# Optimization experiments

Measured on AMD Instinct MI355X. Metric: run time of the kernel, lower is better.

Reference implementation:

```python
import jax, jax.numpy as jnp
import numpy as np
import math

EMBED = 64
HEADS = 2
HEAD_DIM = EMBED // HEADS
B = 262144
EPS = 1e-5


def _linear_params(key, fan_in, fan_out):
    kw, kb = jax.random.split(key)
    bound = 1.0 / math.sqrt(fan_in)
    W = jax.random.uniform(kw, (fan_out, fan_in), jnp.float32, -bound, bound)
    b = jax.random.uniform(kb, (fan_out,), jnp.float32, -bound, bound)
    return W, b


def setup_inputs() -> dict:
    key = jax.random.key(0)
    ks = jax.random.split(key, 12)
    v1 = jax.random.normal(ks[0], (B, EMBED), jnp.float32)
    v2 = jax.random.normal(ks[1], (B, EMBED), jnp.float32)
    Wq1, bq1 = _linear_params(ks[2], EMBED, EMBED)
    Wk2, bk2 = _linear_params(ks[3], EMBED, EMBED)
    Wv2, bv2 = _linear_params(ks[4], EMBED, EMBED)
    Wo1, bo1 = _linear_params(ks[5], EMBED, EMBED)
    Wq2, bq2 = _linear_params(ks[6], EMBED, EMBED)
    Wk1, bk1 = _linear_params(ks[7], EMBED, EMBED)
    Wv1, bv1 = _linear_params(ks[8], EMBED, EMBED)
    Wo2, bo2 = _linear_params(ks[9], EMBED, EMBED)
    g1 = jnp.ones((EMBED,), jnp.float32); be1 = jnp.zeros((EMBED,), jnp.float32)
    g2 = jnp.ones((EMBED,), jnp.float32); be2 = jnp.zeros((EMBED,), jnp.float32)
    return dict(v1_embed=v1, v2_embed=v2,
                Wq1=Wq1, bq1=bq1, Wk2=Wk2, bk2=bk2, Wv2=Wv2, bv2=bv2, Wo1=Wo1, bo1=bo1,
                Wq2=Wq2, bq2=bq2, Wk1=Wk1, bk1=bk1, Wv1=Wv1, bv1=bv1, Wo2=Wo2, bo2=bo2,
                g1=g1, be1=be1, g2=g2, be2=be2)


def _lin(x, W, b):
    return x @ W.T + b


def _mha_single_token(q, k, v):
    # q,k,v: (B, EMBED); one query token, one key token per batch element.
    Bq = q.shape[0]
    Q = q.reshape(Bq, HEADS, HEAD_DIM)
    K = k.reshape(Bq, HEADS, HEAD_DIM)
    V = v.reshape(Bq, HEADS, HEAD_DIM)
    scores = jnp.sum(Q * K, axis=-1, keepdims=True) / jnp.sqrt(jnp.float32(HEAD_DIM))  # (B,H,1)
    w = jax.nn.softmax(scores[..., None], axis=-1)[..., 0]  # softmax over length-1 key axis -> 1.0
    attended = w * V  # (B,H,HEAD_DIM)
    return attended.reshape(Bq, EMBED)


def _layernorm(x, g, b):
    mu = jnp.mean(x, axis=-1, keepdims=True)
    var = jnp.mean(jnp.square(x - mu), axis=-1, keepdims=True)
    return (x - mu) * jax.lax.rsqrt(var + EPS) * g + b


def reference(v1_embed, v2_embed, Wq1, bq1, Wk2, bk2, Wv2, bv2, Wo1, bo1,
              Wq2, bq2, Wk1, bk1, Wv1, bv1, Wo2, bo2, g1, be1, g2, be2):
    # v1 attends to v2
    q1p = _lin(v1_embed, Wq1, bq1)
    k2p = _lin(v2_embed, Wk2, bk2)
    v2p = _lin(v2_embed, Wv2, bv2)
    a1 = _lin(_mha_single_token(q1p, k2p, v2p), Wo1, bo1)
    a1 = _layernorm(a1 + v1_embed, g1, be1)
    # v2 attends to v1
    q2p = _lin(v2_embed, Wq2, bq2)
    k1p = _lin(v1_embed, Wk1, bk1)
    v1p = _lin(v1_embed, Wv1, bv1)
    a2 = _lin(_mha_single_token(q2p, k1p, v1p), Wo2, bo2)
    a2 = _layernorm(a2 + v2_embed, g2, be2)
    return a1, a2
```

## Files before the change

### kernel.cpp

```cpp
#include <hip/hip_runtime.h>

typedef unsigned short u16;
typedef short v8s __attribute__((ext_vector_type(8)));
typedef float f4 __attribute__((ext_vector_type(4)));

#define NROWS 262144
#define UNITS 4

__device__ __forceinline__ u16 f2bf(float f) {
  union { float f; unsigned int i; } x; x.f = f;
  unsigned int r = x.i + 0x7fffu + ((x.i >> 16) & 1u);
  return (u16)(r >> 16);
}

__global__ void fuse_weights(const float* __restrict__ Wo1, const float* __restrict__ Wv2,
                             const float* __restrict__ bv2, const float* __restrict__ bo1,
                             const float* __restrict__ Wo2, const float* __restrict__ Wv1,
                             const float* __restrict__ bv1, const float* __restrict__ bo2,
                             const float* __restrict__ g1,  const float* __restrict__ be1,
                             const float* __restrict__ g2,  const float* __restrict__ be2,
                             u16* __restrict__ M1, u16* __restrict__ M2,
                             float* __restrict__ cgb) {
  int item = blockIdx.x * 256 + threadIdx.x;
  int mat = item >> 10;
  int n   = (item >> 4) & 63;
  int k0  = (item & 15) * 4;
  const float* Wo = mat ? Wo2 : Wo1;
  const float* Wv = mat ? Wv1 : Wv2;
  float a0 = 0.f, a1 = 0.f, a2 = 0.f, a3 = 0.f;
  for (int j = 0; j < 64; ++j) {
    float w = Wo[n * 64 + j];
    f4 wv = *(const f4*)(Wv + j * 64 + k0);
    a0 += w * wv[0];
    a1 += w * wv[1];
    a2 += w * wv[2];
    a3 += w * wv[3];
  }
  u16* M = mat ? M2 : M1;
  M[n * 64 + k0 + 0] = f2bf(a0);
  M[n * 64 + k0 + 1] = f2bf(a1);
  M[n * 64 + k0 + 2] = f2bf(a2);
  M[n * 64 + k0 + 3] = f2bf(a3);
  if ((item & 15) == 0) {
    const float* bv = mat ? bv1 : bv2;
    const float* bo = mat ? bo2 : bo1;
    float s = bo[n];
    for (int j = 0; j < 64; ++j) s += Wo[n * 64 + j] * bv[j];
    cgb[mat * 64 + n] = s;
    const float* g  = mat ? g2 : g1;
    const float* be = mat ? be2 : be1;
    cgb[128 + mat * 128 + n] = g[n];
    cgb[192 + mat * 128 + n] = be[n];
  }
}

__global__ __launch_bounds__(256, 3) void xattn(
    const float* __restrict__ v1, const float* __restrict__ v2,
    const u16* __restrict__ M1, const u16* __restrict__ M2,
    const float* __restrict__ cgb,
    float* __restrict__ out1, float* __restrict__ out2) {
  const int lane = threadIdx.x & 63;
  const int wave = threadIdx.x >> 6;
  const int quad = lane >> 4;
  const int l15  = lane & 15;
  const int path = wave & 1;

  __shared__ float scgb[384];
  if (threadIdx.x < 96)
    ((f4*)scgb)[threadIdx.x] = ((const f4*)cgb)[threadIdx.x];

  const u16*   M    = path ? M2  : M1;
  const float* xsrc = path ? v1  : v2;
  const float* rsrc = path ? v2  : v1;
  float*       outp = path ? out2 : out1;
  const int coff = path * 64;
  const int goff = 128 + path * 128;
  const int boff = 192 + path * 128;

  v8s a[4][2];
#pragma unroll
  for (int mt = 0; mt < 4; ++mt)
#pragma unroll
    for (int ks = 0; ks < 2; ++ks)
      a[mt][ks] = *(const v8s*)(M + (mt * 16 + l15) * 64 + ks * 32 + quad * 8);

  const int unit0 = blockIdx.x * 2 + (wave >> 1);

  f4 x0[2], x1[2], x2[2], x3[2];
  f4 rv0[2], rv1[2], rv2[2], rv3[2];

  auto stage = [&](int buf, int tile) {
    const int rr = tile * 16;
    const float* xrow = xsrc + (size_t)(rr + l15) * 64 + quad * 8;
    x0[buf] = *(const f4*)(xrow);
    x1[buf] = *(const f4*)(xrow + 4);
    x2[buf] = *(const f4*)(xrow + 32);
    x3[buf] = *(const f4*)(xrow + 36);
    const float* rrow = rsrc + (size_t)(rr + l15) * 64 + quad * 4;
    rv0[buf] = *(const f4*)(rrow);
    rv1[buf] = *(const f4*)(rrow + 16);
    rv2[buf] = *(const f4*)(rrow + 32);
    rv3[buf] = *(const f4*)(rrow + 48);
  };

  stage(0, unit0);
  __syncthreads();

#pragma unroll
  for (int it = 0; it < UNITS; ++it) {
    const int cur = it & 1;
    const int nxt = cur ^ 1;
    const int r0 = (unit0 + it * 4096) * 16;

    if (it + 1 < UNITS) stage(nxt, unit0 + (it + 1) * 4096);

    v8s b0, b1;
#pragma unroll
    for (int j = 0; j < 4; ++j) {
      b0[j]     = (short)f2bf(x0[cur][j]);
      b0[j + 4] = (short)f2bf(x1[cur][j]);
      b1[j]     = (short)f2bf(x2[cur][j]);
      b1[j + 4] = (short)f2bf(x3[cur][j]);
    }

    f4 acc[4];
#pragma unroll
    for (int mt = 0; mt < 4; ++mt) {
      f4 c = {0.f, 0.f, 0.f, 0.f};
      c = __builtin_amdgcn_mfma_f32_16x16x32_bf16(a[mt][0], b0, c, 0, 0, 0);
      c = __builtin_amdgcn_mfma_f32_16x16x32_bf16(a[mt][1], b1, c, 0, 0, 0);
      acc[mt] = c;
    }

    float sum = 0.f, sq = 0.f;
#pragma unroll
    for (int mt = 0; mt < 4; ++mt) {
      const int fo = mt * 16 + quad * 4;
      f4 cf = *(const f4*)(scgb + coff + fo);
      f4 rr = mt == 0 ? rv0[cur] : mt == 1 ? rv1[cur] : mt == 2 ? rv2[cur] : rv3[cur];
#pragma unroll
      for (int j = 0; j < 4; ++j) {
        float t = acc[mt][j] + cf[j] + rr[j];
        acc[mt][j] = t;
        sum += t;
        sq  += t * t;
      }
    }
    sum += __shfl_xor(sum, 16, 64);
    sq  += __shfl_xor(sq,  16, 64);
    sum += __shfl_xor(sum, 32, 64);
    sq  += __shfl_xor(sq,  32, 64);
    float mean = sum * 0.015625f;
    float var  = sq * 0.015625f - mean * mean;
    float rstd = rsqrtf(var + 1e-5f);

    float* orow = outp + (size_t)(r0 + l15) * 64 + quad * 4;
#pragma unroll
    for (int mt = 0; mt < 4; ++mt) {
      const int fo = mt * 16 + quad * 4;
      f4 g  = *(const f4*)(scgb + goff + fo);
      f4 be = *(const f4*)(scgb + boff + fo);
      f4 o;
#pragma unroll
      for (int j = 0; j < 4; ++j)
        o[j] = (acc[mt][j] - mean) * rstd * g[j] + be[j];
      *(f4*)(orow + mt * 16) = o;
    }
  }
}

extern "C" void kernel_launch(void* const* d_in, const int* in_sizes, int n_in,
                              void* d_out, int out_size, void* d_ws, size_t ws_size,
                              hipStream_t stream) {
  const float* v1  = (const float*)d_in[0];
  const float* v2  = (const float*)d_in[1];
  const float* Wv2 = (const float*)d_in[6];
  const float* bv2 = (const float*)d_in[7];
  const float* Wo1 = (const float*)d_in[8];
  const float* bo1 = (const float*)d_in[9];
  const float* Wv1 = (const float*)d_in[14];
  const float* bv1 = (const float*)d_in[15];
  const float* Wo2 = (const float*)d_in[16];
  const float* bo2 = (const float*)d_in[17];
  const float* g1  = (const float*)d_in[18];
  const float* be1 = (const float*)d_in[19];
  const float* g2  = (const float*)d_in[20];
  const float* be2 = (const float*)d_in[21];

  u16* M1 = (u16*)d_ws;
  u16* M2 = M1 + 4096;
  float* cgb = (float*)((char*)d_ws + 16384);

  float* out1 = (float*)d_out;
  float* out2 = out1 + (size_t)NROWS * 64;

  fuse_weights<<<8, 256, 0, stream>>>(Wo1, Wv2, bv2, bo1, Wo2, Wv1, bv1, bo2,
                                      g1, be1, g2, be2, M1, M2, cgb);
  xattn<<<2048, 256, 0, stream>>>(v1, v2, M1, M2, cgb, out1, out2);
}
```

Baseline: 297.6 us.

## Stage input tiles via async global-to-LDS loads with double buffering

Input rows for each wave are now copied directly from global memory into per-wave LDS double buffers using global_load_lds, with manual vmcnt waits, instead of being loaded into registers. The grid is halved and each block processes twice as many tiles (UNITS 8, stride 2048), with launch bounds lowered to 2. The intent is to make the loads fully coalesced and free registers for deeper prefetching. The cost is 64KB of LDS per block, which limits occupancy, and correctness depends on the hand-written waitcnt counts.

```diff
diff --git a/kernel.cpp b/kernel.cpp
--- a/kernel.cpp
+++ b/kernel.cpp
@@ -5,13 +5,23 @@
 typedef float f4 __attribute__((ext_vector_type(4)));
 
 #define NROWS 262144
-#define UNITS 4
+#define UNITS 8
+#define TSTRIDE 2048
 
 __device__ __forceinline__ u16 f2bf(float f) {
   union { float f; unsigned int i; } x; x.f = f;
   unsigned int r = x.i + 0x7fffu + ((x.i >> 16) & 1u);
   return (u16)(r >> 16);
 }
+
+typedef const __attribute__((address_space(1))) float* gp1;
+typedef __attribute__((address_space(3))) float* lp3;
+__device__ __forceinline__ void g2l16(const float* g, float* l) {
+  __builtin_amdgcn_global_load_lds((gp1)g, (lp3)l, 16, 0, 0);
+}
+
+#define FENCE_LGKM0() asm volatile("s_waitcnt lgkmcnt(0)" ::: "memory")
+#define FENCE_VM(n)   asm volatile("s_waitcnt vmcnt(" #n ")" ::: "memory")
 
 __global__ void fuse_weights(const float* __restrict__ Wo1, const float* __restrict__ Wv2,
                              const float* __restrict__ bv2, const float* __restrict__ bo1,
@@ -54,7 +64,7 @@
   }
 }
 
-__global__ __launch_bounds__(256, 3) void xattn(
+__global__ __launch_bounds__(256, 2) void xattn(
     const float* __restrict__ v1, const float* __restrict__ v2,
     const u16* __restrict__ M1, const u16* __restrict__ M2,
     const float* __restrict__ cgb,
@@ -65,6 +75,7 @@
   const int l15  = lane & 15;
   const int path = wave & 1;
 
+  __shared__ float sbuf[4][2][2][1024];
   __shared__ float scgb[384];
   if (threadIdx.x < 96)
     ((f4*)scgb)[threadIdx.x] = ((const f4*)cgb)[threadIdx.x];
@@ -77,6 +88,8 @@
   const int goff = 128 + path * 128;
   const int boff = 192 + path * 128;
 
+  __syncthreads();
+
   v8s a[4][2];
 #pragma unroll
   for (int mt = 0; mt < 4; ++mt)
@@ -86,41 +99,55 @@
 
   const int unit0 = blockIdx.x * 2 + (wave >> 1);
 
-  f4 x0[2], x1[2], x2[2], x3[2];
-  f4 rv0[2], rv1[2], rv2[2], rv3[2];
+  const int soff = (lane >> 4) * 64 + (lane & 15) * 4;
 
   auto stage = [&](int buf, int tile) {
-    const int rr = tile * 16;
-    const float* xrow = xsrc + (size_t)(rr + l15) * 64 + quad * 8;
-    x0[buf] = *(const f4*)(xrow);
-    x1[buf] = *(const f4*)(xrow + 4);
-    x2[buf] = *(const f4*)(xrow + 32);
-    x3[buf] = *(const f4*)(xrow + 36);
-    const float* rrow = rsrc + (size_t)(rr + l15) * 64 + quad * 4;
-    rv0[buf] = *(const f4*)(rrow);
-    rv1[buf] = *(const f4*)(rrow + 16);
-    rv2[buf] = *(const f4*)(rrow + 32);
-    rv3[buf] = *(const f4*)(rrow + 48);
+    const size_t rbase = (size_t)tile * 16;
+    const float* xg = xsrc + rbase * 64 + soff;
+    const float* rg = rsrc + rbase * 64 + soff;
+    float* xl = &sbuf[wave][buf][0][0];
+    float* rl = &sbuf[wave][buf][1][0];
+#pragma unroll
+    for (int j = 0; j < 4; ++j) {
+      g2l16(xg + j * 256, xl + j * 256);
+      g2l16(rg + j * 256, rl + j * 256);
+    }
   };
 
   stage(0, unit0);
-  __syncthreads();
+  stage(1, unit0 + TSTRIDE);
 
 #pragma unroll
   for (int it = 0; it < UNITS; ++it) {
-    const int cur = it & 1;
-    const int nxt = cur ^ 1;
-    const int r0 = (unit0 + it * 4096) * 16;
-
-    if (it + 1 < UNITS) stage(nxt, unit0 + (it + 1) * 4096);
+    const int buf = it & 1;
+
+    if (it > 0 && it + 1 < UNITS) {
+      FENCE_LGKM0();
+      stage(buf ^ 1, unit0 + (it + 1) * TSTRIDE);
+    }
+
+    if (it == 0)              { FENCE_VM(8); }
+    else if (it == UNITS - 1) { FENCE_VM(4); }
+    else                      { FENCE_VM(12); }
+
+    const float* xw = &sbuf[wave][buf][0][0];
+    const float* rw = &sbuf[wave][buf][1][0];
+    f4 x0 = *(const f4*)(xw + l15 * 64 + quad * 8);
+    f4 x1 = *(const f4*)(xw + l15 * 64 + quad * 8 + 4);
+    f4 x2 = *(const f4*)(xw + l15 * 64 + quad * 8 + 32);
+    f4 x3 = *(const f4*)(xw + l15 * 64 + quad * 8 + 36);
+    f4 rv[4];
+#pragma unroll
+    for (int mt = 0; mt < 4; ++mt)
+      rv[mt] = *(const f4*)(rw + l15 * 64 + mt * 16 + quad * 4);
 
     v8s b0, b1;
 #pragma unroll
     for (int j = 0; j < 4; ++j) {
-      b0[j]     = (short)f2bf(x0[cur][j]);
-      b0[j + 4] = (short)f2bf(x1[cur][j]);
-      b1[j]     = (short)f2bf(x2[cur][j]);
-      b1[j + 4] = (short)f2bf(x3[cur][j]);
+      b0[j]     = (short)f2bf(x0[j]);
+      b0[j + 4] = (short)f2bf(x1[j]);
+      b1[j]     = (short)f2bf(x2[j]);
+      b1[j + 4] = (short)f2bf(x3[j]);
     }
 
     f4 acc[4];
@@ -137,10 +164,9 @@
     for (int mt = 0; mt < 4; ++mt) {
       const int fo = mt * 16 + quad * 4;
       f4 cf = *(const f4*)(scgb + coff + fo);
-      f4 rr = mt == 0 ? rv0[cur] : mt == 1 ? rv1[cur] : mt == 2 ? rv2[cur] : rv3[cur];
 #pragma unroll
       for (int j = 0; j < 4; ++j) {
-        float t = acc[mt][j] + cf[j] + rr[j];
+        float t = acc[mt][j] + cf[j] + rv[mt][j];
         acc[mt][j] = t;
         sum += t;
         sq  += t * t;
@@ -154,7 +180,8 @@
     float var  = sq * 0.015625f - mean * mean;
     float rstd = rsqrtf(var + 1e-5f);
 
-    float* orow = outp + (size_t)(r0 + l15) * 64 + quad * 4;
+    const size_t r0 = (size_t)(unit0 + it * TSTRIDE) * 16;
+    float* orow = outp + (r0 + l15) * 64 + quad * 4;
 #pragma unroll
     for (int mt = 0; mt < 4; ++mt) {
       const int fo = mt * 16 + quad * 4;
@@ -196,5 +223,5 @@
 
   fuse_weights<<<8, 256, 0, stream>>>(Wo1, Wv2, bv2, bo1, Wo2, Wv1, bv1, bo2,
                                       g1, be1, g2, be2, M1, M2, cgb);
-  xattn<<<2048, 256, 0, stream>>>(v1, v2, M1, M2, cgb, out1, out2);
-}
+  xattn<<<1024, 256, 0, stream>>>(v1, v2, M1, M2, cgb, out1, out2);
+}
```

After: 281.9 us. 1.06x faster.
